# Performance work log

Measured on AMD Instinct MI355X. Metric: run time of the kernel, lower is better.

Reference implementation:

```python
import jax, jax.numpy as jnp
import numpy as np

N = 100000   # nodes
E = 1600000  # edges (avg degree 16)
IN, H, OUT = 64, 128, 1


def setup_inputs() -> dict:
    key = jax.random.key(0)
    ks = jax.random.split(key, 12)
    s = 0.05
    return {
        "x": jax.random.normal(ks[0], (N, IN), jnp.float32),
        "edge_index": jax.random.randint(ks[1], (2, E), 0, N, dtype=jnp.int64),
        "Wl1": jax.random.normal(ks[2], (IN, H), jnp.float32) * s,
        "Wr1": jax.random.normal(ks[3], (IN, H), jnp.float32) * s,
        "b1": jnp.zeros((H,), jnp.float32),
        "ln_g": jnp.ones((H,), jnp.float32),
        "ln_b": jnp.zeros((H,), jnp.float32),
        "Wres": jax.random.normal(ks[4], (IN, H), jnp.float32) * s,
        "bres": jnp.zeros((H,), jnp.float32),
        "Wl2": jax.random.normal(ks[5], (H, H), jnp.float32) * s,
        "Wr2": jax.random.normal(ks[6], (H, H), jnp.float32) * s,
        "b2": jnp.zeros((H,), jnp.float32),
        "Wl3": jax.random.normal(ks[7], (H, H), jnp.float32) * s,
        "Wr3": jax.random.normal(ks[8], (H, H), jnp.float32) * s,
        "b3": jnp.zeros((H,), jnp.float32),
        "Wl4": jax.random.normal(ks[9], (H, OUT), jnp.float32) * s,
        "Wr4": jax.random.normal(ks[10], (H, OUT), jnp.float32) * s,
        "b4": jnp.zeros((OUT,), jnp.float32),
    }


def _sage(h, src, dst, deg_inv, Wl, Wr, b):
    # PyG SAGEConv, aggr='mean': lin_l(mean_{j in N(i)} h_j) + lin_r(h_i)
    agg = jax.ops.segment_sum(h[src], dst, num_segments=N) * deg_inv[:, None]
    return agg @ Wl + h @ Wr + b


def _layernorm(h, g, b, eps=1e-5):
    mu = jnp.mean(h, axis=-1, keepdims=True)
    var = jnp.mean((h - mu) ** 2, axis=-1, keepdims=True)
    return (h - mu) * jax.lax.rsqrt(var + eps) * g + b


def reference(x, edge_index, Wl1, Wr1, b1, ln_g, ln_b, Wres, bres,
              Wl2, Wr2, b2, Wl3, Wr3, b3, Wl4, Wr4, b4):
    src, dst = edge_index[0], edge_index[1]
    deg = jax.ops.segment_sum(jnp.ones((E,), jnp.float32), dst, num_segments=N)
    deg_inv = 1.0 / jnp.maximum(deg, 1.0)

    h = jax.nn.relu(_layernorm(_sage(x, src, dst, deg_inv, Wl1, Wr1, b1), ln_g, ln_b))
    h = h + x @ Wres + bres              # residual (in_channel != hidden_channel)
    h = jax.nn.relu(_sage(h, src, dst, deg_inv, Wl2, Wr2, b2))   # dropout: eval no-op
    h = jax.nn.relu(_sage(h, src, dst, deg_inv, Wl3, Wr3, b3))
    out = _sage(h, src, dst, deg_inv, Wl4, Wr4, b4)
    return out.squeeze(-1)
```

## Files before the change

kernel.cpp:

```cpp
#include <hip/hip_runtime.h>
#include <hip/hip_bf16.h>

#define N_NODES 100000
#define N_EDGES 1600000

#define NBKT 782
#define SCAT_BLOCKS 240
#define BKT_CHUNK 6667

#define SORT_BLOCKS 40
#define SORT_CHUNK 2500
#define BH2_N (NBKT * SCAT_BLOCKS)
#define BHB ((BH2_N + 1023) / 1024)
#define XBF_BLOCKS 6250

#define NSTRIPS 6250
#define GEMM_BLOCKS 782

typedef __attribute__((ext_vector_type(8))) short short8v;
typedef __attribute__((ext_vector_type(4))) float float4v;

__device__ __forceinline__ unsigned short f2bf(float f) {
    unsigned int u = __float_as_uint(f);
    u = (u + 0x7FFFu + ((u >> 16) & 1u)) >> 16;
    return (unsigned short)u;
}
__device__ __forceinline__ float bf2f(unsigned short b) {
    return __uint_as_float((unsigned int)b << 16);
}

typedef __attribute__((address_space(1))) const unsigned int gld_g_t;
typedef __attribute__((address_space(3))) unsigned int gld_l_t;
__device__ __forceinline__ void gld_lds16(const void* g, void* l) {
    __builtin_amdgcn_global_load_lds((gld_g_t*)g, (gld_l_t*)l, 16, 0, 0);
}

#define SWZ128(row, ksh) ((row) * 128 + ((ksh) ^ (((row) & 7) << 3)))
#define SWZ256(row, ksh) ((row) * 256 + ((ksh) ^ (((row) & 7) << 3)))

__global__ __launch_bounds__(256) void hist_xbf_kernel(const int* __restrict__ ei, int* __restrict__ bh2,
                                                       const float* __restrict__ x, unsigned short* __restrict__ xsrc) {
    __shared__ int h[NBKT];
    int tid = threadIdx.x;
    if (blockIdx.x < SCAT_BLOCKS) {
        for (int i = tid; i < NBKT; i += 256) h[i] = 0;
        __syncthreads();
        int start = blockIdx.x * BKT_CHUNK;
        int end = start + BKT_CHUNK; if (end > N_EDGES) end = N_EDGES;
        for (int i = start + tid; i < end; i += 256) {
            int d = ei[N_EDGES + i];
            atomicAdd(&h[d >> 7], 1);
        }
        __syncthreads();
        for (int i = tid; i < NBKT; i += 256) bh2[i * SCAT_BLOCKS + blockIdx.x] = h[i];
    } else {
        int idx = (blockIdx.x - SCAT_BLOCKS) * 256 + tid;
        if (idx < N_NODES * 16) {
            int node = idx >> 4;
            int f0 = (idx & 15) * 4;
            float4 v = *(const float4*)(x + (size_t)idx * 4);
            ushort4 o;
            o.x = f2bf(v.x); o.y = f2bf(v.y); o.z = f2bf(v.z); o.w = f2bf(v.w);
            *(ushort4*)(xsrc + (size_t)node * 64 + f0) = o;
        }
    }
}

__global__ __launch_bounds__(256) void gscan_a_kernel(const int* __restrict__ in, int* __restrict__ bsum, int n) {
    __shared__ int lds[256];
    int tid = threadIdx.x;
    int base = blockIdx.x * 1024 + tid * 4;
    int s = 0;
    #pragma unroll
    for (int i = 0; i < 4; i++) s += (base + i < n) ? in[base + i] : 0;
    lds[tid] = s;
    __syncthreads();
    for (int off = 128; off; off >>= 1) {
        if (tid < off) lds[tid] += lds[tid + off];
        __syncthreads();
    }
    if (tid == 0) bsum[blockIdx.x] = lds[0];
}

__global__ __launch_bounds__(256) void gscan_c_kernel(int* __restrict__ data, const int* __restrict__ bsum,
                                                      int nb, int n) {
    __shared__ int sb[256];
    __shared__ int lds[256];
    int tid = threadIdx.x;
    sb[tid] = (tid < nb) ? bsum[tid] : 0;
    __syncthreads();
    for (int off = 1; off < 256; off <<= 1) {
        int y = 0;
        if (tid >= off) y = sb[tid - off];
        __syncthreads();
        if (tid >= off) sb[tid] += y;
        __syncthreads();
    }
    int blockbase = (blockIdx.x == 0) ? 0 : sb[blockIdx.x - 1];

    int base = blockIdx.x * 1024 + tid * 4;
    int v[4];
    int s = 0;
    #pragma unroll
    for (int i = 0; i < 4; i++) {
        v[i] = (base + i < n) ? data[base + i] : 0;
        s += v[i];
    }
    lds[tid] = s;
    __syncthreads();
    for (int off = 1; off < 256; off <<= 1) {
        int y = 0;
        if (tid >= off) y = lds[tid - off];
        __syncthreads();
        if (tid >= off) lds[tid] += y;
        __syncthreads();
    }
    int run = blockbase + lds[tid] - s;
    #pragma unroll
    for (int i = 0; i < 4; i++) {
        if (base + i < n) data[base + i] = run;
        run += v[i];
    }
}

__global__ __launch_bounds__(256) void bkt_scatter2_kernel(const int* __restrict__ ei, const int* __restrict__ bh2,
                                                           int* __restrict__ packed) {
    __shared__ int h[NBKT];
    __shared__ int base[NBKT];
    int tid = threadIdx.x;
    for (int i = tid; i < NBKT; i += 256) { h[i] = 0; base[i] = bh2[i * SCAT_BLOCKS + blockIdx.x]; }
    __syncthreads();
    int start = blockIdx.x * BKT_CHUNK;
    int end = start + BKT_CHUNK; if (end > N_EDGES) end = N_EDGES;
    for (int i = start + tid; i < end; i += 256) {
        int s = ei[i];
        int d = ei[N_EDGES + i];
        int b = d >> 7;
        int pos = base[b] + atomicAdd(&h[b], 1);
        packed[pos] = (s << 7) | (d & 127);
    }
}

__global__ __launch_bounds__(256) void bkt_build_kernel(const int* __restrict__ packed, const int* __restrict__ bh2,
                                                        int* __restrict__ deg, int* __restrict__ row_ptr,
                                                        int* __restrict__ col) {
    __shared__ int c[128];
    __shared__ int rp[128];
    int tid = threadIdx.x;
    int s0 = bh2[blockIdx.x * SCAT_BLOCKS];
    int s1 = (blockIdx.x + 1 < NBKT) ? bh2[(blockIdx.x + 1) * SCAT_BLOCKS] : N_EDGES;
    if (tid < 128) c[tid] = 0;
    __syncthreads();
    for (int i = s0 + tid; i < s1; i += 256) atomicAdd(&c[packed[i] & 127], 1);
    __syncthreads();
    if (tid < 128) rp[tid] = c[tid];
    __syncthreads();
    for (int off = 1; off < 128; off <<= 1) {
        int y = 0;
        if (tid >= off && tid < 128) y = rp[tid - off];
        __syncthreads();
        if (tid >= off && tid < 128) rp[tid] += y;
        __syncthreads();
    }
    int node = blockIdx.x * 128 + tid;
    if (tid < 128) {
        rp[tid] = s0 + rp[tid] - c[tid];
        if (node < N_NODES) {
            deg[node] = c[tid];
            row_ptr[node] = rp[tid];
        }
        c[tid] = 0;
    }
    if (blockIdx.x == 0 && tid == 0) row_ptr[N_NODES] = N_EDGES;
    __syncthreads();
    for (int i = s0 + tid; i < s1; i += 256) {
        int p = packed[i];
        int dl = p & 127;
        int pos = rp[dl] + atomicAdd(&c[dl], 1);
        col[pos] = p >> 7;
    }
}

__global__ __launch_bounds__(256) void dsort_hist_kernel(const int* __restrict__ deg, int* __restrict__ bh) {
    __shared__ int h[64];
    int tid = threadIdx.x;
    if (tid < 64) h[tid] = 0;
    __syncthreads();
    int start = blockIdx.x * SORT_CHUNK;
    int end = start + SORT_CHUNK; if (end > N_NODES) end = N_NODES;
    for (int i = start + tid; i < end; i += 256) atomicAdd(&h[63 - min(deg[i], 63)], 1);
    __syncthreads();
    if (tid < 64) bh[tid * SORT_BLOCKS + blockIdx.x] = h[tid];
}

__global__ __launch_bounds__(256) void dsort_scat_kernel(const int* __restrict__ deg, const int* __restrict__ bh,
                                                         int* __restrict__ ord) {
    __shared__ int sbh[64 * SORT_BLOCKS];
    __shared__ int ps[256];
    __shared__ int h[64];
    int tid = threadIdx.x;
    int v[10];
    int s = 0;
    #pragma unroll
    for (int k = 0; k < 10; k++) { v[k] = bh[tid * 10 + k]; s += v[k]; }
    ps[tid] = s;
    if (tid < 64) h[tid] = 0;
    __syncthreads();
    for (int off = 1; off < 256; off <<= 1) {
        int y = 0;
        if (tid >= off) y = ps[tid - off];
        __syncthreads();
        if (tid >= off) ps[tid] += y;
        __syncthreads();
    }
    int run = ps[tid] - s;
    #pragma unroll
    for (int k = 0; k < 10; k++) { sbh[tid * 10 + k] = run; run += v[k]; }
    __syncthreads();
    int start = blockIdx.x * SORT_CHUNK;
    int end = start + SORT_CHUNK; if (end > N_NODES) end = N_NODES;
    for (int i = start + tid; i < end; i += 256) {
        int b = 63 - min(deg[i], 63);
        int pos = sbh[b * SORT_BLOCKS + blockIdx.x] + atomicAdd(&h[b], 1);
        ord[pos] = i;
    }
}

#define ACC4(u) { a0 += bf2f(u.x); a1 += bf2f(u.y); a2 += bf2f(u.z); a3 += bf2f(u.w); }

__global__ __launch_bounds__(256) void agg64_kernel(const unsigned short* __restrict__ xsrc,
                                                    unsigned short* __restrict__ aggx,
                                                    const int* __restrict__ row_ptr, const int* __restrict__ col,
                                                    const int* __restrict__ ord) {
    int tid = threadIdx.x;
    int slot = blockIdx.x * 16 + (tid >> 4);
    if (slot >= N_NODES) return;
    int i = ord[slot];
    int f0 = (tid & 15) * 4;
    int s = row_ptr[i], e = row_ptr[i + 1];
    float a0 = 0.f, a1 = 0.f, a2 = 0.f, a3 = 0.f;
    int t = s;
    while (t + 7 < e) {
        int j0 = col[t], j1 = col[t + 1], j2 = col[t + 2], j3 = col[t + 3];
        int j4 = col[t + 4], j5 = col[t + 5], j6 = col[t + 6], j7 = col[t + 7];
        ushort4 u0 = *(const ushort4*)(xsrc + (size_t)j0 * 64 + f0);
        ushort4 u1 = *(const ushort4*)(xsrc + (size_t)j1 * 64 + f0);
        ushort4 u2 = *(const ushort4*)(xsrc + (size_t)j2 * 64 + f0);
        ushort4 u3 = *(const ushort4*)(xsrc + (size_t)j3 * 64 + f0);
        ushort4 u4 = *(const ushort4*)(xsrc + (size_t)j4 * 64 + f0);
        ushort4 u5 = *(const ushort4*)(xsrc + (size_t)j5 * 64 + f0);
        ushort4 u6 = *(const ushort4*)(xsrc + (size_t)j6 * 64 + f0);
        ushort4 u7 = *(const ushort4*)(xsrc + (size_t)j7 * 64 + f0);
        ACC4(u0) ACC4(u1) ACC4(u2) ACC4(u3) ACC4(u4) ACC4(u5) ACC4(u6) ACC4(u7)
        t += 8;
    }
    if (t + 3 < e) {
        int j0 = col[t], j1 = col[t + 1], j2 = col[t + 2], j3 = col[t + 3];
        ushort4 u0 = *(const ushort4*)(xsrc + (size_t)j0 * 64 + f0);
        ushort4 u1 = *(const ushort4*)(xsrc + (size_t)j1 * 64 + f0);
        ushort4 u2 = *(const ushort4*)(xsrc + (size_t)j2 * 64 + f0);
        ushort4 u3 = *(const ushort4*)(xsrc + (size_t)j3 * 64 + f0);
        ACC4(u0) ACC4(u1) ACC4(u2) ACC4(u3)
        t += 4;
    }
    if (t + 1 < e) {
        int j0 = col[t], j1 = col[t + 1];
        ushort4 u0 = *(const ushort4*)(xsrc + (size_t)j0 * 64 + f0);
        ushort4 u1 = *(const ushort4*)(xsrc + (size_t)j1 * 64 + f0);
        ACC4(u0) ACC4(u1)
        t += 2;
    }
    if (t < e) {
        ushort4 u0 = *(const ushort4*)(xsrc + (size_t)col[t] * 64 + f0);
        ACC4(u0)
    }
    float di = 1.0f / fmaxf((float)(e - s), 1.0f);
    ushort4 o;
    o.x = f2bf(a0 * di); o.y = f2bf(a1 * di); o.z = f2bf(a2 * di); o.w = f2bf(a3 * di);
    *(ushort4*)(aggx + (size_t)i * 64 + f0) = o;
}

__global__ __launch_bounds__(256) void agg128_kernel(const unsigned short* __restrict__ hsrc,
                                                     unsigned short* __restrict__ aggh,
                                                     const int* __restrict__ row_ptr, const int* __restrict__ col,
                                                     const int* __restrict__ ord) {
    int tid = threadIdx.x;
    int slot = blockIdx.x * 8 + (tid >> 5);
    if (slot >= N_NODES) return;
    int i = ord[slot];
    int f0 = (tid & 31) * 4;
    int s = row_ptr[i], e = row_ptr[i + 1];
    float a0 = 0.f, a1 = 0.f, a2 = 0.f, a3 = 0.f;
    int t = s;
    while (t + 7 < e) {
        int j0 = col[t], j1 = col[t + 1], j2 = col[t + 2], j3 = col[t + 3];
        int j4 = col[t + 4], j5 = col[t + 5], j6 = col[t + 6], j7 = col[t + 7];
        ushort4 u0 = *(const ushort4*)(hsrc + (size_t)j0 * 128 + f0);
        ushort4 u1 = *(const ushort4*)(hsrc + (size_t)j1 * 128 + f0);
        ushort4 u2 = *(const ushort4*)(hsrc + (size_t)j2 * 128 + f0);
        ushort4 u3 = *(const ushort4*)(hsrc + (size_t)j3 * 128 + f0);
        ushort4 u4 = *(const ushort4*)(hsrc + (size_t)j4 * 128 + f0);
        ushort4 u5 = *(const ushort4*)(hsrc + (size_t)j5 * 128 + f0);
        ushort4 u6 = *(const ushort4*)(hsrc + (size_t)j6 * 128 + f0);
        ushort4 u7 = *(const ushort4*)(hsrc + (size_t)j7 * 128 + f0);
        ACC4(u0) ACC4(u1) ACC4(u2) ACC4(u3) ACC4(u4) ACC4(u5) ACC4(u6) ACC4(u7)
        t += 8;
    }
    if (t + 3 < e) {
        int j0 = col[t], j1 = col[t + 1], j2 = col[t + 2], j3 = col[t + 3];
        ushort4 u0 = *(const ushort4*)(hsrc + (size_t)j0 * 128 + f0);
        ushort4 u1 = *(const ushort4*)(hsrc + (size_t)j1 * 128 + f0);
        ushort4 u2 = *(const ushort4*)(hsrc + (size_t)j2 * 128 + f0);
        ushort4 u3 = *(const ushort4*)(hsrc + (size_t)j3 * 128 + f0);
        ACC4(u0) ACC4(u1) ACC4(u2) ACC4(u3)
        t += 4;
    }
    if (t + 1 < e) {
        int j0 = col[t], j1 = col[t + 1];
        ushort4 u0 = *(const ushort4*)(hsrc + (size_t)j0 * 128 + f0);
        ushort4 u1 = *(const ushort4*)(hsrc + (size_t)j1 * 128 + f0);
        ACC4(u0) ACC4(u1)
        t += 2;
    }
    if (t < e) {
        ushort4 u0 = *(const ushort4*)(hsrc + (size_t)col[t] * 128 + f0);
        ACC4(u0)
    }
    float di = 1.0f / fmaxf((float)(e - s), 1.0f);
    ushort4 o;
    o.x = f2bf(a0 * di); o.y = f2bf(a1 * di); o.z = f2bf(a2 * di); o.w = f2bf(a3 * di);
    *(ushort4*)(aggh + (size_t)i * 128 + f0) = o;
}

__global__ __launch_bounds__(256) void wprep_all_kernel(const float* __restrict__ Wr1, const float* __restrict__ Wl1,
                                                        const float* __restrict__ Wres,
                                                        const float* __restrict__ Wl2, const float* __restrict__ Wr2,
                                                        const float* __restrict__ Wl3, const float* __restrict__ Wr3,
                                                        unsigned short* __restrict__ Bt1,
                                                        unsigned short* __restrict__ Bt2,
                                                        unsigned short* __restrict__ Bt3) {
    int idx = blockIdx.x * 256 + threadIdx.x;
    int seg = idx >> 15;
    int loc = idx & 32767;
    if (seg == 0) {
        int n = loc >> 7;
        int k = loc & 127;
        float v;
        if (n < 128) v = (k < 64) ? Wr1[k * 128 + n] : Wl1[(k - 64) * 128 + n];
        else         v = (k < 64) ? Wres[k * 128 + (n - 128)] : 0.f;
        Bt1[loc] = f2bf(v);
    } else if (seg == 1) {
        int n = loc >> 8;
        int k = loc & 255;
        float v = (k < 128) ? Wr2[k * 128 + n] : Wl2[(k - 128) * 128 + n];
        Bt2[loc] = f2bf(v);
    } else if (seg == 2) {
        int n = loc >> 8;
        int k = loc & 255;
        float v = (k < 128) ? Wr3[k * 128 + n] : Wl3[(k - 128) * 128 + n];
        Bt3[loc] = f2bf(v);
    }
}

__global__ __launch_bounds__(512) void mgemm1_ln_kernel(const unsigned short* __restrict__ Ax,
                                                        const unsigned short* __restrict__ Aa,
                                                        const unsigned short* __restrict__ Bt,
                                                        const float* __restrict__ b1, const float* __restrict__ ln_g,
                                                        const float* __restrict__ ln_b, const float* __restrict__ bres,
                                                        unsigned short* __restrict__ hsrc) {
    __shared__ unsigned short Bs[32768];
    int tid = threadIdx.x;
    int wave = tid >> 6, lane = tid & 63;
    int lm = lane & 15, lk = (lane >> 4) * 8;

    #pragma unroll
    for (int rnd = 0; rnd < 8; rnd++) {
        int Lb = rnd * 8192 + tid * 16;
        int row = Lb >> 8;
        int sb = (Lb & 255) ^ ((row & 7) << 4);
        gld_lds16(Bt + (size_t)row * 128 + (sb >> 1), &Bs[Lb >> 1]);
    }
    __syncthreads();

    int strip = blockIdx.x * 8 + wave;
    if (strip >= NSTRIPS) return;
    int m0 = strip * 16;

    float4v accT[8], accR[8];
    #pragma unroll
    for (int j = 0; j < 8; j++) { accT[j] = (float4v)0.f; accR[j] = (float4v)0.f; }

    const unsigned short* arx = Ax + (size_t)(m0 + lm) * 64 + lk;
    const unsigned short* ara = Aa + (size_t)(m0 + lm) * 64 + lk;
    #pragma unroll
    for (int k0 = 0; k0 < 128; k0 += 32) {
        short8v af = (k0 < 64) ? *(const short8v*)(arx + k0) : *(const short8v*)(ara + (k0 - 64));
        short8v bf[8];
        #pragma unroll
        for (int j = 0; j < 8; j++)
            bf[j] = *(const short8v*)&Bs[SWZ128(j * 16 + lm, k0 + lk)];
        #pragma unroll
        for (int j = 0; j < 8; j++)
            accT[j] = __builtin_amdgcn_mfma_f32_16x16x32_bf16(af, bf[j], accT[j], 0, 0, 0);
        if (k0 < 64) {
            short8v bg[8];
            #pragma unroll
            for (int j = 0; j < 8; j++)
                bg[j] = *(const short8v*)&Bs[SWZ128(128 + j * 16 + lm, k0 + lk)];
            #pragma unroll
            for (int j = 0; j < 8; j++)
                accR[j] = __builtin_amdgcn_mfma_f32_16x16x32_bf16(af, bg[j], accR[j], 0, 0, 0);
        }
    }

    float b1v[8], gv[8], bbv[8], brv[8];
    #pragma unroll
    for (int j = 0; j < 8; j++) {
        int cc = j * 16 + lm;
        b1v[j] = b1[cc]; gv[j] = ln_g[cc]; bbv[j] = ln_b[cc]; brv[j] = bres[cc];
    }
    int q4 = lane >> 4;
    #pragma unroll
    for (int r = 0; r < 4; r++) {
        float sp = 0.f, sq = 0.f;
        #pragma unroll
        for (int j = 0; j < 8; j++) {
            float tv = accT[j][r] + b1v[j];
            sp += tv; sq += tv * tv;
        }
        #pragma unroll
        for (int off = 1; off < 16; off <<= 1) {
            sp += __shfl_xor(sp, off);
            sq += __shfl_xor(sq, off);
        }
        float mu = sp * (1.f / 128.f);
        float var = sq * (1.f / 128.f) - mu * mu;
        float rstd = rsqrtf(var + 1e-5f);
        int gm = m0 + q4 * 4 + r;
        #pragma unroll
        for (int j = 0; j < 8; j++) {
            float tv = accT[j][r] + b1v[j];
            float y = fmaxf((tv - mu) * rstd * gv[j] + bbv[j], 0.f) + accR[j][r] + brv[j];
            hsrc[(size_t)gm * 128 + j * 16 + lm] = f2bf(y);
        }
    }
}

__global__ __launch_bounds__(512) void mgemm_kernel(const unsigned short* __restrict__ Ah,
                                                    const unsigned short* __restrict__ Aa,
                                                    const unsigned short* __restrict__ Bt,
                                                    const float* __restrict__ bias,
                                                    unsigned short* __restrict__ C) {
    __shared__ unsigned short Bs[32768];
    int tid = threadIdx.x;
    int wave = tid >> 6, lane = tid & 63;
    int lm = lane & 15, lk = (lane >> 4) * 8;

    #pragma unroll
    for (int rnd = 0; rnd < 8; rnd++) {
        int Lb = rnd * 8192 + tid * 16;
        int row = Lb >> 9;
        int sb = (Lb & 511) ^ ((row & 7) << 4);
        gld_lds16(Bt + ((size_t)row << 8) + (sb >> 1), &Bs[Lb >> 1]);
    }
    __syncthreads();

    int strip = blockIdx.x * 8 + wave;
    if (strip >= NSTRIPS) return;
    int m0 = strip * 16;

    float4v acc[8];
    #pragma unroll
    for (int j = 0; j < 8; j++) acc[j] = (float4v)0.f;

    const unsigned short* arh = Ah + (size_t)(m0 + lm) * 128 + lk;
    const unsigned short* ara = Aa + (size_t)(m0 + lm) * 128 + lk;
    #pragma unroll
    for (int k0 = 0; k0 < 256; k0 += 32) {
        short8v af = (k0 < 128) ? *(const short8v*)(arh + k0) : *(const short8v*)(ara + (k0 - 128));
        short8v bf[8];
        #pragma unroll
        for (int j = 0; j < 8; j++)
            bf[j] = *(const short8v*)&Bs[SWZ256(j * 16 + lm, k0 + lk)];
        #pragma unroll
        for (int j = 0; j < 8; j++)
            acc[j] = __builtin_amdgcn_mfma_f32_16x16x32_bf16(af, bf[j], acc[j], 0, 0, 0);
    }

    int q4 = lane >> 4;
    #pragma unroll
    for (int j = 0; j < 8; j++) {
        int cc = j * 16 + lm;
        float bv = bias[cc];
        #pragma unroll
        for (int r = 0; r < 4; r++) {
            int m = m0 + q4 * 4 + r;
            C[(size_t)m * 128 + cc] = f2bf(fmaxf(acc[j][r] + bv, 0.f));
        }
    }
}

__global__ __launch_bounds__(512) void mgemm_pq_kernel(const unsigned short* __restrict__ Ah,
                                                       const unsigned short* __restrict__ Aa,
                                                       const unsigned short* __restrict__ Bt,
                                                       const float* __restrict__ bias,
                                                       const float* __restrict__ Wl4, const float* __restrict__ Wr4,
                                                       const float* __restrict__ b4,
                                                       float* __restrict__ p, float* __restrict__ q) {
    __shared__ unsigned short Bs[32768];
    int tid = threadIdx.x;
    int wave = tid >> 6, lane = tid & 63;
    int lm = lane & 15, lk = (lane >> 4) * 8;

    #pragma unroll
    for (int rnd = 0; rnd < 8; rnd++) {
        int Lb = rnd * 8192 + tid * 16;
        int row = Lb >> 9;
        int sb = (Lb & 511) ^ ((row & 7) << 4);
        gld_lds16(Bt + ((size_t)row << 8) + (sb >> 1), &Bs[Lb >> 1]);
    }
    __syncthreads();

    int strip = blockIdx.x * 8 + wave;
    if (strip >= NSTRIPS) return;
    int m0 = strip * 16;

    float4v acc[8];
    #pragma unroll
    for (int j = 0; j < 8; j++) acc[j] = (float4v)0.f;

    const unsigned short* arh = Ah + (size_t)(m0 + lm) * 128 + lk;
    const unsigned short* ara = Aa + (size_t)(m0 + lm) * 128 + lk;
    #pragma unroll
    for (int k0 = 0; k0 < 256; k0 += 32) {
        short8v af = (k0 < 128) ? *(const short8v*)(arh + k0) : *(const short8v*)(ara + (k0 - 128));
        short8v bf[8];
        #pragma unroll
        for (int j = 0; j < 8; j++)
            bf[j] = *(const short8v*)&Bs[SWZ256(j * 16 + lm, k0 + lk)];
        #pragma unroll
        for (int j = 0; j < 8; j++)
            acc[j] = __builtin_amdgcn_mfma_f32_16x16x32_bf16(af, bf[j], acc[j], 0, 0, 0);
    }

    float b3v[8], wlv[8], wrv[8];
    #pragma unroll
    for (int j = 0; j < 8; j++) {
        int cc = j * 16 + lm;
        b3v[j] = bias[cc]; wlv[j] = Wl4[cc]; wrv[j] = Wr4[cc];
    }
    float b4v = b4[0];
    int q4 = lane >> 4;
    #pragma unroll
    for (int r = 0; r < 4; r++) {
        float pp = 0.f, qq = 0.f;
        #pragma unroll
        for (int j = 0; j < 8; j++) {
            float hv = fmaxf(acc[j][r] + b3v[j], 0.f);
            pp += hv * wlv[j]; qq += hv * wrv[j];
        }
        #pragma unroll
        for (int off = 1; off < 16; off <<= 1) {
            pp += __shfl_xor(pp, off);
            qq += __shfl_xor(qq, off);
        }
        if (lm == 0) {
            int m = m0 + q4 * 4 + r;
            p[m] = pp;
            q[m] = qq + b4v;
        }
    }
}

__global__ __launch_bounds__(256) void final_kernel(const float* __restrict__ p, const float* __restrict__ q,
                                                    const int* __restrict__ row_ptr, const int* __restrict__ col,
                                                    float* __restrict__ out) {
    int i = blockIdx.x * 256 + threadIdx.x;
    if (i >= N_NODES) return;
    int s = row_ptr[i], e = row_ptr[i + 1];
    float acc = 0.f;
    int t = s;
    for (; t + 7 < e; t += 8)
        acc += p[col[t]] + p[col[t + 1]] + p[col[t + 2]] + p[col[t + 3]]
             + p[col[t + 4]] + p[col[t + 5]] + p[col[t + 6]] + p[col[t + 7]];
    for (; t < e; t++) acc += p[col[t]];
    float di = 1.0f / fmaxf((float)(e - s), 1.0f);
    out[i] = acc * di + q[i];
}


extern "C" void kernel_launch(void* const* d_in, const int* in_sizes, int n_in,
                              void* d_out, int out_size, void* d_ws, size_t ws_size,
                              hipStream_t stream) {
    const float* x    = (const float*)d_in[0];
    const int*   ei   = (const int*)d_in[1];
    const float* Wl1  = (const float*)d_in[2];
    const float* Wr1  = (const float*)d_in[3];
    const float* b1   = (const float*)d_in[4];
    const float* ln_g = (const float*)d_in[5];
    const float* ln_b = (const float*)d_in[6];
    const float* Wres = (const float*)d_in[7];
    const float* bres = (const float*)d_in[8];
    const float* Wl2  = (const float*)d_in[9];
    const float* Wr2  = (const float*)d_in[10];
    const float* b2   = (const float*)d_in[11];
    const float* Wl3  = (const float*)d_in[12];
    const float* Wr3  = (const float*)d_in[13];
    const float* b3   = (const float*)d_in[14];
    const float* Wl4  = (const float*)d_in[15];
    const float* Wr4  = (const float*)d_in[16];
    const float* b4   = (const float*)d_in[17];
    float* out = (float*)d_out;

    char* w = (char*)d_ws;
    size_t off = 0;
    auto alloc = [&](size_t bytes) -> void* {
        off = (off + 255) & ~(size_t)255;
        void* pp = w + off;
        off += bytes;
        return pp;
    };

    int*   deg        = (int*)alloc(N_NODES * 4);
    int*   row_ptr    = (int*)alloc((N_NODES + 1) * 4);
    int*   bsum       = (int*)alloc(1024);
    int*   col        = (int*)alloc(N_EDGES * 4);
    int*   bh2        = (int*)alloc(BH2_N * 4);
    int*   bh         = (int*)alloc(64 * SORT_BLOCKS * 4);
    int*   ord        = (int*)alloc(N_NODES * 4);
    unsigned short* Bt1  = (unsigned short*)alloc(256 * 128 * 2);
    unsigned short* Bt2  = (unsigned short*)alloc(128 * 256 * 2);
    unsigned short* Bt3  = (unsigned short*)alloc(128 * 256 * 2);
    unsigned short* xsrc = (unsigned short*)alloc((size_t)N_NODES * 64 * 2);
    unsigned short* aggx = (unsigned short*)alloc((size_t)N_NODES * 64 * 2);
    unsigned short* hsrc = (unsigned short*)alloc((size_t)N_NODES * 128 * 2);
    unsigned short* aggh = (unsigned short*)alloc((size_t)N_NODES * 128 * 2);
    int*   packed  = (int*)alloc((size_t)N_EDGES * 4);
    float* p       = (float*)alloc(N_NODES * 4);
    float* q       = (float*)alloc(N_NODES * 4);
    (void)ws_size; (void)n_in; (void)in_sizes; (void)out_size;

    const int NB = (N_NODES + 255) / 256;

    wprep_all_kernel<<<384, 256, 0, stream>>>(Wr1, Wl1, Wres, Wl2, Wr2, Wl3, Wr3, Bt1, Bt2, Bt3);

    hist_xbf_kernel<<<SCAT_BLOCKS + XBF_BLOCKS, 256, 0, stream>>>(ei, bh2, x, xsrc);
    gscan_a_kernel<<<BHB, 256, 0, stream>>>(bh2, bsum, BH2_N);
    gscan_c_kernel<<<BHB, 256, 0, stream>>>(bh2, bsum, BHB, BH2_N);
    bkt_scatter2_kernel<<<SCAT_BLOCKS, 256, 0, stream>>>(ei, bh2, packed);
    bkt_build_kernel<<<NBKT, 256, 0, stream>>>(packed, bh2, deg, row_ptr, col);
    dsort_hist_kernel<<<SORT_BLOCKS, 256, 0, stream>>>(deg, bh);
    dsort_scat_kernel<<<SORT_BLOCKS, 256, 0, stream>>>(deg, bh, ord);

    agg64_kernel<<<(N_NODES + 15) / 16, 256, 0, stream>>>(xsrc, aggx, row_ptr, col, ord);
    mgemm1_ln_kernel<<<GEMM_BLOCKS, 512, 0, stream>>>(xsrc, aggx, Bt1, b1, ln_g, ln_b, bres, hsrc);

    agg128_kernel<<<(N_NODES + 7) / 8, 256, 0, stream>>>(hsrc, aggh, row_ptr, col, ord);
    mgemm_kernel<<<GEMM_BLOCKS, 512, 0, stream>>>(hsrc, aggh, Bt2, b2, hsrc);

    agg128_kernel<<<(N_NODES + 7) / 8, 256, 0, stream>>>(hsrc, aggh, row_ptr, col, ord);
    mgemm_pq_kernel<<<GEMM_BLOCKS, 512, 0, stream>>>(hsrc, aggh, Bt3, b3, Wl4, Wr4, b4, p, q);

    final_kernel<<<NB, 256, 0, stream>>>(p, q, row_ptr, col, out);
}
```

Baseline: 368.2 us.

## Fuse neighbor mean aggregation into the MFMA GEMM kernels

Removes the separate agg64/agg128 kernels and has each GEMM lane gather its node's neighbors (in degree-sorted order) directly into registers, feeding the aggregated bf16 row straight into the MFMA A operand. This avoids writing and re-reading the aggx/aggh intermediate buffers and drops three launches. The weight load into LDS now overlaps with the gather. A ping-pong buffer h2 is added because in-place writes would race with other blocks' gathers. In exchange, each lane walks a whole neighbor list with 16-byte loads, so per-wave parallelism over the gather is lower and blocks mixing different degrees may show load imbalance.

```diff
diff --git a/kernel.cpp b/kernel.cpp
--- a/kernel.cpp
+++ b/kernel.cpp
@@ -14,8 +14,7 @@
 #define BHB ((BH2_N + 1023) / 1024)
 #define XBF_BLOCKS 6250
 
-#define NSTRIPS 6250
-#define GEMM_BLOCKS 782
+#define FG_BLOCKS 782
 
 typedef __attribute__((ext_vector_type(8))) short short8v;
 typedef __attribute__((ext_vector_type(4))) float float4v;
@@ -37,6 +36,18 @@
 
 #define SWZ128(row, ksh) ((row) * 128 + ((ksh) ^ (((row) & 7) << 3)))
 #define SWZ256(row, ksh) ((row) * 256 + ((ksh) ^ (((row) & 7) << 3)))
+
+#define GACC(u, A, B) { A[0] += bf2f((unsigned short)u[0]); A[1] += bf2f((unsigned short)u[1]); \
+                        A[2] += bf2f((unsigned short)u[2]); A[3] += bf2f((unsigned short)u[3]); \
+                        B[0] += bf2f((unsigned short)u[4]); B[1] += bf2f((unsigned short)u[5]); \
+                        B[2] += bf2f((unsigned short)u[6]); B[3] += bf2f((unsigned short)u[7]); }
+
+__device__ __forceinline__ short8v pack_bf(const float4v lo, const float4v hi, float di) {
+    short8v r;
+    r[0] = f2bf(lo[0] * di); r[1] = f2bf(lo[1] * di); r[2] = f2bf(lo[2] * di); r[3] = f2bf(lo[3] * di);
+    r[4] = f2bf(hi[0] * di); r[5] = f2bf(hi[1] * di); r[6] = f2bf(hi[2] * di); r[7] = f2bf(hi[3] * di);
+    return r;
+}
 
 __global__ __launch_bounds__(256) void hist_xbf_kernel(const int* __restrict__ ei, int* __restrict__ bh2,
                                                        const float* __restrict__ x, unsigned short* __restrict__ xsrc) {
@@ -224,112 +235,6 @@
         int pos = sbh[b * SORT_BLOCKS + blockIdx.x] + atomicAdd(&h[b], 1);
         ord[pos] = i;
     }
-}
-
-#define ACC4(u) { a0 += bf2f(u.x); a1 += bf2f(u.y); a2 += bf2f(u.z); a3 += bf2f(u.w); }
-
-__global__ __launch_bounds__(256) void agg64_kernel(const unsigned short* __restrict__ xsrc,
-                                                    unsigned short* __restrict__ aggx,
-                                                    const int* __restrict__ row_ptr, const int* __restrict__ col,
-                                                    const int* __restrict__ ord) {
-    int tid = threadIdx.x;
-    int slot = blockIdx.x * 16 + (tid >> 4);
-    if (slot >= N_NODES) return;
-    int i = ord[slot];
-    int f0 = (tid & 15) * 4;
-    int s = row_ptr[i], e = row_ptr[i + 1];
-    float a0 = 0.f, a1 = 0.f, a2 = 0.f, a3 = 0.f;
-    int t = s;
-    while (t + 7 < e) {
-        int j0 = col[t], j1 = col[t + 1], j2 = col[t + 2], j3 = col[t + 3];
-        int j4 = col[t + 4], j5 = col[t + 5], j6 = col[t + 6], j7 = col[t + 7];
-        ushort4 u0 = *(const ushort4*)(xsrc + (size_t)j0 * 64 + f0);
-        ushort4 u1 = *(const ushort4*)(xsrc + (size_t)j1 * 64 + f0);
-        ushort4 u2 = *(const ushort4*)(xsrc + (size_t)j2 * 64 + f0);
-        ushort4 u3 = *(const ushort4*)(xsrc + (size_t)j3 * 64 + f0);
-        ushort4 u4 = *(const ushort4*)(xsrc + (size_t)j4 * 64 + f0);
-        ushort4 u5 = *(const ushort4*)(xsrc + (size_t)j5 * 64 + f0);
-        ushort4 u6 = *(const ushort4*)(xsrc + (size_t)j6 * 64 + f0);
-        ushort4 u7 = *(const ushort4*)(xsrc + (size_t)j7 * 64 + f0);
-        ACC4(u0) ACC4(u1) ACC4(u2) ACC4(u3) ACC4(u4) ACC4(u5) ACC4(u6) ACC4(u7)
-        t += 8;
-    }
-    if (t + 3 < e) {
-        int j0 = col[t], j1 = col[t + 1], j2 = col[t + 2], j3 = col[t + 3];
-        ushort4 u0 = *(const ushort4*)(xsrc + (size_t)j0 * 64 + f0);
-        ushort4 u1 = *(const ushort4*)(xsrc + (size_t)j1 * 64 + f0);
-        ushort4 u2 = *(const ushort4*)(xsrc + (size_t)j2 * 64 + f0);
-        ushort4 u3 = *(const ushort4*)(xsrc + (size_t)j3 * 64 + f0);
-        ACC4(u0) ACC4(u1) ACC4(u2) ACC4(u3)
-        t += 4;
-    }
-    if (t + 1 < e) {
-        int j0 = col[t], j1 = col[t + 1];
-        ushort4 u0 = *(const ushort4*)(xsrc + (size_t)j0 * 64 + f0);
-        ushort4 u1 = *(const ushort4*)(xsrc + (size_t)j1 * 64 + f0);
-        ACC4(u0) ACC4(u1)
-        t += 2;
-    }
-    if (t < e) {
-        ushort4 u0 = *(const ushort4*)(xsrc + (size_t)col[t] * 64 + f0);
-        ACC4(u0)
-    }
-    float di = 1.0f / fmaxf((float)(e - s), 1.0f);
-    ushort4 o;
-    o.x = f2bf(a0 * di); o.y = f2bf(a1 * di); o.z = f2bf(a2 * di); o.w = f2bf(a3 * di);
-    *(ushort4*)(aggx + (size_t)i * 64 + f0) = o;
-}
-
-__global__ __launch_bounds__(256) void agg128_kernel(const unsigned short* __restrict__ hsrc,
-                                                     unsigned short* __restrict__ aggh,
-                                                     const int* __restrict__ row_ptr, const int* __restrict__ col,
-                                                     const int* __restrict__ ord) {
-    int tid = threadIdx.x;
-    int slot = blockIdx.x * 8 + (tid >> 5);
-    if (slot >= N_NODES) return;
-    int i = ord[slot];
-    int f0 = (tid & 31) * 4;
-    int s = row_ptr[i], e = row_ptr[i + 1];
-    float a0 = 0.f, a1 = 0.f, a2 = 0.f, a3 = 0.f;
-    int t = s;
-    while (t + 7 < e) {
-        int j0 = col[t], j1 = col[t + 1], j2 = col[t + 2], j3 = col[t + 3];
-        int j4 = col[t + 4], j5 = col[t + 5], j6 = col[t + 6], j7 = col[t + 7];
-        ushort4 u0 = *(const ushort4*)(hsrc + (size_t)j0 * 128 + f0);
-        ushort4 u1 = *(const ushort4*)(hsrc + (size_t)j1 * 128 + f0);
-        ushort4 u2 = *(const ushort4*)(hsrc + (size_t)j2 * 128 + f0);
-        ushort4 u3 = *(const ushort4*)(hsrc + (size_t)j3 * 128 + f0);
-        ushort4 u4 = *(const ushort4*)(hsrc + (size_t)j4 * 128 + f0);
-        ushort4 u5 = *(const ushort4*)(hsrc + (size_t)j5 * 128 + f0);
-        ushort4 u6 = *(const ushort4*)(hsrc + (size_t)j6 * 128 + f0);
-        ushort4 u7 = *(const ushort4*)(hsrc + (size_t)j7 * 128 + f0);
-        ACC4(u0) ACC4(u1) ACC4(u2) ACC4(u3) ACC4(u4) ACC4(u5) ACC4(u6) ACC4(u7)
-        t += 8;
-    }
-    if (t + 3 < e) {
-        int j0 = col[t], j1 = col[t + 1], j2 = col[t + 2], j3 = col[t + 3];
-        ushort4 u0 = *(const ushort4*)(hsrc + (size_t)j0 * 128 + f0);
-        ushort4 u1 = *(const ushort4*)(hsrc + (size_t)j1 * 128 + f0);
-        ushort4 u2 = *(const ushort4*)(hsrc + (size_t)j2 * 128 + f0);
-        ushort4 u3 = *(const ushort4*)(hsrc + (size_t)j3 * 128 + f0);
-        ACC4(u0) ACC4(u1) ACC4(u2) ACC4(u3)
-        t += 4;
-    }
-    if (t + 1 < e) {
-        int j0 = col[t], j1 = col[t + 1];
-        ushort4 u0 = *(const ushort4*)(hsrc + (size_t)j0 * 128 + f0);
-        ushort4 u1 = *(const ushort4*)(hsrc + (size_t)j1 * 128 + f0);
-        ACC4(u0) ACC4(u1)
-        t += 2;
-    }
-    if (t < e) {
-        ushort4 u0 = *(const ushort4*)(hsrc + (size_t)col[t] * 128 + f0);
-        ACC4(u0)
-    }
-    float di = 1.0f / fmaxf((float)(e - s), 1.0f);
-    ushort4 o;
-    o.x = f2bf(a0 * di); o.y = f2bf(a1 * di); o.z = f2bf(a2 * di); o.w = f2bf(a3 * di);
-    *(ushort4*)(aggh + (size_t)i * 128 + f0) = o;
 }
 
 __global__ __launch_bounds__(256) void wprep_all_kernel(const float* __restrict__ Wr1, const float* __restrict__ Wl1,
@@ -362,9 +267,10 @@
     }
 }
 
-__global__ __launch_bounds__(512) void mgemm1_ln_kernel(const unsigned short* __restrict__ Ax,
-                                                        const unsigned short* __restrict__ Aa,
+__global__ __launch_bounds__(512) void fgemm1_ln_kernel(const unsigned short* __restrict__ xsrc,
                                                         const unsigned short* __restrict__ Bt,
+                                                        const int* __restrict__ row_ptr, const int* __restrict__ col,
+                                                        const int* __restrict__ ord,
                                                         const float* __restrict__ b1, const float* __restrict__ ln_g,
                                                         const float* __restrict__ ln_b, const float* __restrict__ bres,
                                                         unsigned short* __restrict__ hsrc) {
@@ -380,36 +286,63 @@
         int sb = (Lb & 255) ^ ((row & 7) << 4);
         gld_lds16(Bt + (size_t)row * 128 + (sb >> 1), &Bs[Lb >> 1]);
     }
-    __syncthreads();
-
-    int strip = blockIdx.x * 8 + wave;
-    if (strip >= NSTRIPS) return;
-    int m0 = strip * 16;
+
+    int slot = blockIdx.x * 128 + wave * 16 + lm;
+    if (slot >= N_NODES) slot = N_NODES - 1;
+    int i = ord[slot];
+    int rs = row_ptr[i], re = row_ptr[i + 1];
+
+    short8v ad0 = *(const short8v*)(xsrc + (size_t)i * 64 + lk);
+    short8v ad1 = *(const short8v*)(xsrc + (size_t)i * 64 + 32 + lk);
+
+    float4v a0 = (float4v)0.f, a1 = (float4v)0.f, a2 = (float4v)0.f, a3 = (float4v)0.f;
+    const unsigned short* xb = xsrc + lk;
+    int t = rs;
+    for (; t + 3 < re; t += 4) {
+        int j0 = col[t], j1 = col[t + 1], j2 = col[t + 2], j3 = col[t + 3];
+        short8v u0 = *(const short8v*)(xb + (size_t)j0 * 64);
+        short8v v0 = *(const short8v*)(xb + (size_t)j0 * 64 + 32);
+        short8v u1 = *(const short8v*)(xb + (size_t)j1 * 64);
+        short8v v1 = *(const short8v*)(xb + (size_t)j1 * 64 + 32);
+        short8v u2 = *(const short8v*)(xb + (size_t)j2 * 64);
+        short8v v2 = *(const short8v*)(xb + (size_t)j2 * 64 + 32);
+        short8v u3 = *(const short8v*)(xb + (size_t)j3 * 64);
+        short8v v3 = *(const short8v*)(xb + (size_t)j3 * 64 + 32);
+        GACC(u0, a0, a1) GACC(v0, a2, a3)
+        GACC(u1, a0, a1) GACC(v1, a2, a3)
+        GACC(u2, a0, a1) GACC(v2, a2, a3)
+        GACC(u3, a0, a1) GACC(v3, a2, a3)
+    }
+    for (; t < re; t++) {
+        int j0 = col[t];
+        short8v u0 = *(const short8v*)(xb + (size_t)j0 * 64);
+        short8v v0 = *(const short8v*)(xb + (size_t)j0 * 64 + 32);
+        GACC(u0, a0, a1) GACC(v0, a2, a3)
+    }
+    float di = 1.0f / fmaxf((float)(re - rs), 1.0f);
+    short8v ag0 = pack_bf(a0, a1, di);
+    short8v ag1 = pack_bf(a2, a3, di);
+
+    __syncthreads();
 
     float4v accT[8], accR[8];
     #pragma unroll
     for (int j = 0; j < 8; j++) { accT[j] = (float4v)0.f; accR[j] = (float4v)0.f; }
 
-    const unsigned short* arx = Ax + (size_t)(m0 + lm) * 64 + lk;
-    const unsigned short* ara = Aa + (size_t)(m0 + lm) * 64 + lk;
     #pragma unroll
     for (int k0 = 0; k0 < 128; k0 += 32) {
-        short8v af = (k0 < 64) ? *(const short8v*)(arx + k0) : *(const short8v*)(ara + (k0 - 64));
-        short8v bf[8];
-        #pragma unroll
-        for (int j = 0; j < 8; j++)
-            bf[j] = *(const short8v*)&Bs[SWZ128(j * 16 + lm, k0 + lk)];
-        #pragma unroll
-        for (int j = 0; j < 8; j++)
-            accT[j] = __builtin_amdgcn_mfma_f32_16x16x32_bf16(af, bf[j], accT[j], 0, 0, 0);
+        short8v af = (k0 == 0) ? ad0 : (k0 == 32) ? ad1 : (k0 == 64) ? ag0 : ag1;
+        #pragma unroll
+        for (int j = 0; j < 8; j++) {
+            short8v bfv = *(const short8v*)&Bs[SWZ128(j * 16 + lm, k0 + lk)];
+            accT[j] = __builtin_amdgcn_mfma_f32_16x16x32_bf16(af, bfv, accT[j], 0, 0, 0);
+        }
         if (k0 < 64) {
-            short8v bg[8];
             #pragma unroll
-            for (int j = 0; j < 8; j++)
-                bg[j] = *(const short8v*)&Bs[SWZ128(128 + j * 16 + lm, k0 + lk)];
-            #pragma unroll
-            for (int j = 0; j < 8; j++)
-                accR[j] = __builtin_amdgcn_mfma_f32_16x16x32_bf16(af, bg[j], accR[j], 0, 0, 0);
+            for (int j = 0; j < 8; j++) {
+                short8v bg = *(const short8v*)&Bs[SWZ128(128 + j * 16 + lm, k0 + lk)];
+                accR[j] = __builtin_amdgcn_mfma_f32_16x16x32_bf16(af, bg, accR[j], 0, 0, 0);
+            }
         }
     }
 
@@ -436,7 +369,7 @@
         float mu = sp * (1.f / 128.f);
         float var = sq * (1.f / 128.f) - mu * mu;
         float rstd = rsqrtf(var + 1e-5f);
-        int gm = m0 + q4 * 4 + r;
+        int gm = __shfl(i, q4 * 4 + r, 16);
         #pragma unroll
         for (int j = 0; j < 8; j++) {
             float tv = accT[j][r] + b1v[j];
@@ -446,11 +379,16 @@
     }
 }
 
-__global__ __launch_bounds__(512) void mgemm_kernel(const unsigned short* __restrict__ Ah,
-                                                    const unsigned short* __restrict__ Aa,
-                                                    const unsigned short* __restrict__ Bt,
-                                                    const float* __restrict__ bias,
-                                                    unsigned short* __restrict__ C) {
+template <int PQ>
+__global__ __launch_bounds__(512) void fgemm128_kernel(const unsigned short* __restrict__ H,
+                                                       const unsigned short* __restrict__ Bt,
+                                                       const int* __restrict__ row_ptr, const int* __restrict__ col,
+                                                       const int* __restrict__ ord,
+                                                       const float* __restrict__ bias,
+                                                       unsigned short* __restrict__ C,
+                                                       const float* __restrict__ Wl4, const float* __restrict__ Wr4,
+                                                       const float* __restrict__ b4,
+                                                       float* __restrict__ p, float* __restrict__ q) {
     __shared__ unsigned short Bs[32768];
     int tid = threadIdx.x;
     int wave = tid >> 6, lane = tid & 63;
@@ -463,111 +401,104 @@
         int sb = (Lb & 511) ^ ((row & 7) << 4);
         gld_lds16(Bt + ((size_t)row << 8) + (sb >> 1), &Bs[Lb >> 1]);
     }
-    __syncthreads();
-
-    int strip = blockIdx.x * 8 + wave;
-    if (strip >= NSTRIPS) return;
-    int m0 = strip * 16;
+
+    int slot = blockIdx.x * 128 + wave * 16 + lm;
+    if (slot >= N_NODES) slot = N_NODES - 1;
+    int i = ord[slot];
+    int rs = row_ptr[i], re = row_ptr[i + 1];
+
+    short8v ad0 = *(const short8v*)(H + (size_t)i * 128 + lk);
+    short8v ad1 = *(const short8v*)(H + (size_t)i * 128 + 32 + lk);
+    short8v ad2 = *(const short8v*)(H + (size_t)i * 128 + 64 + lk);
+    short8v ad3 = *(const short8v*)(H + (size_t)i * 128 + 96 + lk);
+
+    float4v a0 = (float4v)0.f, a1 = (float4v)0.f, a2 = (float4v)0.f, a3 = (float4v)0.f;
+    float4v a4 = (float4v)0.f, a5 = (float4v)0.f, a6 = (float4v)0.f, a7 = (float4v)0.f;
+    const unsigned short* hb = H + lk;
+    int t = rs;
+    for (; t + 1 < re; t += 2) {
+        int j0 = col[t], j1 = col[t + 1];
+        short8v u0 = *(const short8v*)(hb + (size_t)j0 * 128);
+        short8v u1 = *(const short8v*)(hb + (size_t)j0 * 128 + 32);
+        short8v u2 = *(const short8v*)(hb + (size_t)j0 * 128 + 64);
+        short8v u3 = *(const short8v*)(hb + (size_t)j0 * 128 + 96);
+        short8v w0 = *(const short8v*)(hb + (size_t)j1 * 128);
+        short8v w1 = *(const short8v*)(hb + (size_t)j1 * 128 + 32);
+        short8v w2 = *(const short8v*)(hb + (size_t)j1 * 128 + 64);
+        short8v w3 = *(const short8v*)(hb + (size_t)j1 * 128 + 96);
+        GACC(u0, a0, a1) GACC(u1, a2, a3) GACC(u2, a4, a5) GACC(u3, a6, a7)
+        GACC(w0, a0, a1) GACC(w1, a2, a3) GACC(w2, a4, a5) GACC(w3, a6, a7)
+    }
+    if (t < re) {
+        int j0 = col[t];
+        short8v u0 = *(const short8v*)(hb + (size_t)j0 * 128);
+        short8v u1 = *(const short8v*)(hb + (size_t)j0 * 128 + 32);
+        short8v u2 = *(const short8v*)(hb + (size_t)j0 * 128 + 64);
+        short8v u3 = *(const short8v*)(hb + (size_t)j0 * 128 + 96);
+        GACC(u0, a0, a1) GACC(u1, a2, a3) GACC(u2, a4, a5) GACC(u3, a6, a7)
+    }
+    float di = 1.0f / fmaxf((float)(re - rs), 1.0f);
+    short8v ag0 = pack_bf(a0, a1, di);
+    short8v ag1 = pack_bf(a2, a3, di);
+    short8v ag2 = pack_bf(a4, a5, di);
+    short8v ag3 = pack_bf(a6, a7, di);
+
+    __syncthreads();
 
     float4v acc[8];
     #pragma unroll
     for (int j = 0; j < 8; j++) acc[j] = (float4v)0.f;
 
-    const unsigned short* arh = Ah + (size_t)(m0 + lm) * 128 + lk;
-    const unsigned short* ara = Aa + (size_t)(m0 + lm) * 128 + lk;
     #pragma unroll
     for (int k0 = 0; k0 < 256; k0 += 32) {
-        short8v af = (k0 < 128) ? *(const short8v*)(arh + k0) : *(const short8v*)(ara + (k0 - 128));
-        short8v bf[8];
-        #pragma unroll
-        for (int j = 0; j < 8; j++)
-            bf[j] = *(const short8v*)&Bs[SWZ256(j * 16 + lm, k0 + lk)];
-        #pragma unroll
-        for (int j = 0; j < 8; j++)
-            acc[j] = __builtin_amdgcn_mfma_f32_16x16x32_bf16(af, bf[j], acc[j], 0, 0, 0);
+        short8v af = (k0 == 0) ? ad0 : (k0 == 32) ? ad1 : (k0 == 64) ? ad2 : (k0 == 96) ? ad3
+                   : (k0 == 128) ? ag0 : (k0 == 160) ? ag1 : (k0 == 192) ? ag2 : ag3;
+        #pragma unroll
+        for (int j = 0; j < 8; j++) {
+            short8v bfv = *(const short8v*)&Bs[SWZ256(j * 16 + lm, k0 + lk)];
+            acc[j] = __builtin_amdgcn_mfma_f32_16x16x32_bf16(af, bfv, acc[j], 0, 0, 0);
+        }
     }
 
     int q4 = lane >> 4;
-    #pragma unroll
-    for (int j = 0; j < 8; j++) {
-        int cc = j * 16 + lm;
-        float bv = bias[cc];
+    int gmv[4];
+    #pragma unroll
+    for (int r = 0; r < 4; r++) gmv[r] = __shfl(i, q4 * 4 + r, 16);
+
+    if (PQ == 0) {
+        #pragma unroll
+        for (int j = 0; j < 8; j++) {
+            int cc = j * 16 + lm;
+            float bv = bias[cc];
+            #pragma unroll
+            for (int r = 0; r < 4; r++)
+                C[(size_t)gmv[r] * 128 + cc] = f2bf(fmaxf(acc[j][r] + bv, 0.f));
+        }
+    } else {
+        float b3v[8], wlv[8], wrv[8];
+        #pragma unroll
+        for (int j = 0; j < 8; j++) {
+            int cc = j * 16 + lm;
+            b3v[j] = bias[cc]; wlv[j] = Wl4[cc]; wrv[j] = Wr4[cc];
+        }
+        float b4v = b4[0];
         #pragma unroll
         for (int r = 0; r < 4; r++) {
-            int m = m0 + q4 * 4 + r;
-            C[(size_t)m * 128 + cc] = f2bf(fmaxf(acc[j][r] + bv, 0.f));
-        }
-    }
-}
-
-__global__ __launch_bounds__(512) void mgemm_pq_kernel(const unsigned short* __restrict__ Ah,
-                                                       const unsigned short* __restrict__ Aa,
-                                                       const unsigned short* __restrict__ Bt,
-                                                       const float* __restrict__ bias,
-                                                       const float* __restrict__ Wl4, const float* __restrict__ Wr4,
-                                                       const float* __restrict__ b4,
-                                                       float* __restrict__ p, float* __restrict__ q) {
-    __shared__ unsigned short Bs[32768];
-    int tid = threadIdx.x;
-    int wave = tid >> 6, lane = tid & 63;
-    int lm = lane & 15, lk = (lane >> 4) * 8;
-
-    #pragma unroll
-    for (int rnd = 0; rnd < 8; rnd++) {
-        int Lb = rnd * 8192 + tid * 16;
-        int row = Lb >> 9;
-        int sb = (Lb & 511) ^ ((row & 7) << 4);
-        gld_lds16(Bt + ((size_t)row << 8) + (sb >> 1), &Bs[Lb >> 1]);
-    }
-    __syncthreads();
-
-    int strip = blockIdx.x * 8 + wave;
-    if (strip >= NSTRIPS) return;
-    int m0 = strip * 16;
-
-    float4v acc[8];
-    #pragma unroll
-    for (int j = 0; j < 8; j++) acc[j] = (float4v)0.f;
-
-    const unsigned short* arh = Ah + (size_t)(m0 + lm) * 128 + lk;
-    const unsigned short* ara = Aa + (size_t)(m0 + lm) * 128 + lk;
-    #pragma unroll
-    for (int k0 = 0; k0 < 256; k0 += 32) {
-        short8v af = (k0 < 128) ? *(const short8v*)(arh + k0) : *(const short8v*)(ara + (k0 - 128));
-        short8v bf[8];
-        #pragma unroll
-        for (int j = 0; j < 8; j++)
-            bf[j] = *(const short8v*)&Bs[SWZ256(j * 16 + lm, k0 + lk)];
-        #pragma unroll
-        for (int j = 0; j < 8; j++)
-            acc[j] = __builtin_amdgcn_mfma_f32_16x16x32_bf16(af, bf[j], acc[j], 0, 0, 0);
-    }
-
-    float b3v[8], wlv[8], wrv[8];
-    #pragma unroll
-    for (int j = 0; j < 8; j++) {
-        int cc = j * 16 + lm;
-        b3v[j] = bias[cc]; wlv[j] = Wl4[cc]; wrv[j] = Wr4[cc];
-    }
-    float b4v = b4[0];
-    int q4 = lane >> 4;
-    #pragma unroll
-    for (int r = 0; r < 4; r++) {
-        float pp = 0.f, qq = 0.f;
-        #pragma unroll
-        for (int j = 0; j < 8; j++) {
-            float hv = fmaxf(acc[j][r] + b3v[j], 0.f);
-            pp += hv * wlv[j]; qq += hv * wrv[j];
-        }
-        #pragma unroll
-        for (int off = 1; off < 16; off <<= 1) {
-            pp += __shfl_xor(pp, off);
-            qq += __shfl_xor(qq, off);
-        }
-        if (lm == 0) {
-            int m = m0 + q4 * 4 + r;
-            p[m] = pp;
-            q[m] = qq + b4v;
+            float pp = 0.f, qq = 0.f;
+            #pragma unroll
+            for (int j = 0; j < 8; j++) {
+                float hv = fmaxf(acc[j][r] + b3v[j], 0.f);
+                pp += hv * wlv[j]; qq += hv * wrv[j];
+            }
+            #pragma unroll
+            for (int off = 1; off < 16; off <<= 1) {
+                pp += __shfl_xor(pp, off);
+                qq += __shfl_xor(qq, off);
+            }
+            if (lm == 0) {
+                p[gmv[r]] = pp;
+                q[gmv[r]] = qq + b4v;
+            }
         }
     }
 }
@@ -632,9 +563,8 @@
     unsigned short* Bt2  = (unsigned short*)alloc(128 * 256 * 2);
     unsigned short* Bt3  = (unsigned short*)alloc(128 * 256 * 2);
     unsigned short* xsrc = (unsigned short*)alloc((size_t)N_NODES * 64 * 2);
-    unsigned short* aggx = (unsigned short*)alloc((size_t)N_NODES * 64 * 2);
     unsigned short* hsrc = (unsigned short*)alloc((size_t)N_NODES * 128 * 2);
-    unsigned short* aggh = (unsigned short*)alloc((size_t)N_NODES * 128 * 2);
+    unsigned short* h2   = (unsigned short*)alloc((size_t)N_NODES * 128 * 2);
     int*   packed  = (int*)alloc((size_t)N_EDGES * 4);
     float* p       = (float*)alloc(N_NODES * 4);
     float* q       = (float*)alloc(N_NODES * 4);
@@ -652,14 +582,14 @@
     dsort_hist_kernel<<<SORT_BLOCKS, 256, 0, stream>>>(deg, bh);
     dsort_scat_kernel<<<SORT_BLOCKS, 256, 0, stream>>>(deg, bh, ord);
 
-    agg64_kernel<<<(N_NODES + 15) / 16, 256, 0, stream>>>(xsrc, aggx, row_ptr, col, ord);
-    mgemm1_ln_kernel<<<GEMM_BLOCKS, 512, 0, stream>>>(xsrc, aggx, Bt1, b1, ln_g, ln_b, bres, hsrc);
-
-    agg128_kernel<<<(N_NODES + 7) / 8, 256, 0, stream>>>(hsrc, aggh, row_ptr, col, ord);
-    mgemm_kernel<<<GEMM_BLOCKS, 512, 0, stream>>>(hsrc, aggh, Bt2, b2, hsrc);
-
-    agg128_kernel<<<(N_NODES + 7) / 8, 256, 0, stream>>>(hsrc, aggh, row_ptr, col, ord);
-    mgemm_pq_kernel<<<GEMM_BLOCKS, 512, 0, stream>>>(hsrc, aggh, Bt3, b3, Wl4, Wr4, b4, p, q);
+    fgemm1_ln_kernel<<<FG_BLOCKS, 512, 0, stream>>>(xsrc, Bt1, row_ptr, col, ord,
+                                                    b1, ln_g, ln_b, bres, hsrc);
+
+    fgemm128_kernel<0><<<FG_BLOCKS, 512, 0, stream>>>(hsrc, Bt2, row_ptr, col, ord,
+                                                      b2, h2, nullptr, nullptr, nullptr, nullptr, nullptr);
+
+    fgemm128_kernel<1><<<FG_BLOCKS, 512, 0, stream>>>(h2, Bt3, row_ptr, col, ord,
+                                                      b3, nullptr, Wl4, Wr4, b4, p, q);
 
     final_kernel<<<NB, 256, 0, stream>>>(p, q, row_ptr, col, out);
 }
```

Measured after the change: 388.3 us. 5.5% more time.
